# Kernel tuning notes

Measured on AMD Instinct MI355X. Metric: run time of the kernel, lower is better.

## Reference

```python
import jax, jax.numpy as jnp
import numpy as np
from itertools import product

MAX_ALLOC = [3, 3, 3, 3, 3, 3]   # env.maximum_allocation -> 4^6 = 4096 actions
NUM_SESSIONS = 64
STATE_DIM = NUM_SESSIONS + len(MAX_ALLOC)  # 70
HIDDEN = (1024, 1024)
BATCH = 8192


def setup_inputs() -> dict:
    key = jax.random.key(0)
    ks = jax.random.split(key, 8)
    # states: sessions part uniform [0,1); waitlist part uniform [0,4) so mask is nontrivial
    sessions = jax.random.uniform(ks[0], (BATCH, NUM_SESSIONS), dtype=jnp.float32)
    waitlist = jax.random.uniform(ks[1], (BATCH, len(MAX_ALLOC)), dtype=jnp.float32) * 4.0
    states = jnp.concatenate([sessions, waitlist], axis=1)
    # enumerated action space, same order as itertools.product in the torch module
    action_space = jnp.asarray(
        np.array(list(product(*[range(m + 1) for m in MAX_ALLOC])), dtype=np.int32))  # [4096, 6]
    A = action_space.shape[0]
    W1 = jax.random.normal(ks[2], (STATE_DIM, HIDDEN[0]), dtype=jnp.float32) / np.sqrt(STATE_DIM)
    b1 = jnp.zeros((HIDDEN[0],), dtype=jnp.float32)
    W2 = jax.random.normal(ks[3], (HIDDEN[0], HIDDEN[1]), dtype=jnp.float32) / np.sqrt(HIDDEN[0])
    b2 = jnp.zeros((HIDDEN[1],), dtype=jnp.float32)
    Wh = jax.random.normal(ks[4], (HIDDEN[1], A), dtype=jnp.float32) / np.sqrt(HIDDEN[1])
    bh = jnp.zeros((A,), dtype=jnp.float32)
    return {"states": states, "W1": W1, "b1": b1, "W2": W2, "b2": b2,
            "Wh": Wh, "bh": bh, "action_space": action_space,
            "num_sessions": NUM_SESSIONS}


def reference(states, W1, b1, W2, b2, Wh, bh, action_space, num_sessions):
    # vectorized get_action_mask: action j is feasible for row i iff all(action_j <= waitlist_i)
    waitlist = states[:, num_sessions:]                                   # [B, 6]
    feasible = jnp.all(action_space[None, :, :].astype(states.dtype)
                       <= waitlist[:, None, :], axis=-1)                  # [B, A] bool
    mask = feasible.astype(states.dtype)
    # tanh MLP
    h = jnp.tanh(states @ W1 + b1)
    h = jnp.tanh(h @ W2 + b2)
    logits = h @ Wh + bh + jnp.log(mask + 1e-9)                           # [B, A]
    return jax.nn.softmax(logits, axis=1)
```

## Files before the change

kernel.cpp:

```cpp
#include <hip/hip_runtime.h>
#include <hip/hip_bf16.h>
#include <math.h>

using bf16 = __hip_bfloat16;
typedef __attribute__((ext_vector_type(8))) short short8;
typedef __attribute__((ext_vector_type(4))) float f32x4;
typedef __attribute__((ext_vector_type(4))) unsigned int u32x4;

#define BATCH 8192
#define SDIM  70
#define NS    64
#define HID   1024
#define NA    4096
#define KPAD  128

__device__ __forceinline__ void gld_lds16(const bf16* g, bf16* l) {
    __builtin_amdgcn_global_load_lds(
        (const __attribute__((address_space(1))) void*)g,
        (__attribute__((address_space(3))) void*)l, 16, 0, 0);
}

__device__ __forceinline__ short f2bf(float v) {
    union { bf16 b; short s; } u; u.b = __float2bfloat16(v); return u.s;
}

__device__ __forceinline__ void tr32(const float* __restrict__ in, bf16* __restrict__ out,
                                     int K, int N, int Kpad, int bx, int by, int t,
                                     float (*tile)[33]) {
    int kb = by * 32, nb = bx * 32;
    int tx = t & 31, ty = t >> 5;
    #pragma unroll
    for (int i = 0; i < 32; i += 8) {
        int k = kb + ty + i, n = nb + tx;
        tile[ty + i][tx] = (k < K) ? in[(size_t)k * N + n] : 0.0f;
    }
    __syncthreads();
    #pragma unroll
    for (int i = 0; i < 32; i += 8) {
        int n = nb + ty + i, k = kb + tx;
        if (k < Kpad) out[(size_t)n * Kpad + k] = __float2bfloat16(tile[tx][ty + i]);
    }
}

__global__ __launch_bounds__(256)
void prep_k(const float* __restrict__ states, const float* __restrict__ W1,
            const float* __restrict__ W2, const float* __restrict__ Wh,
            const int* __restrict__ act,
            bf16* __restrict__ statesb, bf16* __restrict__ w1bt,
            bf16* __restrict__ w2bt, bf16* __restrict__ whbt,
            unsigned* __restrict__ pact, unsigned* __restrict__ trow) {
    __shared__ float tile[32][33];
    const int b = blockIdx.x, t = threadIdx.x;
    if (b < 512) {
        int idx = b * 256 + t;
        int row = idx >> 4;
        int c0  = (idx & 15) * 8;
        const float* src = states + (size_t)row * SDIM;
        short8 o;
        #pragma unroll
        for (int i = 0; i < 8; i++) {
            int c = c0 + i;
            o[i] = f2bf((c < SDIM) ? src[c] : 0.0f);
        }
        *(short8*)&statesb[(size_t)row * KPAD + c0] = o;
    } else if (b < 640) {
        int r = b - 512;
        tr32(W1, w1bt, SDIM, HID, KPAD, r & 31, r >> 5, t, tile);
    } else if (b < 1664) {
        int r = b - 640;
        tr32(W2, w2bt, HID, HID, HID, r & 31, r >> 5, t, tile);
    } else if (b < 5760) {
        int r = b - 1664;
        tr32(Wh, whbt, HID, NA, HID, r & 127, r >> 7, t, tile);
    } else if (b < 5776) {
        int c = (b - 5760) * 256 + t;
        if (c < NA) {
            const int* a = act + c * 6;
            unsigned p = 0;
            #pragma unroll
            for (int i = 0; i < 6; i++) p |= ((unsigned)a[i]) << (5 * i);
            pact[c] = p;
        }
    } else {
        int row = (b - 5776) * 256 + t;
        const float* wl = states + (size_t)row * SDIM + NS;
        unsigned T = 0;
        #pragma unroll
        for (int i = 0; i < 6; i++) T |= ((unsigned)(int)wl[i]) << (5 * i);
        trow[row] = T;
    }
}

template<int MODE, int BN>
__global__ __launch_bounds__(256)
void gemm128(const bf16* __restrict__ A, const bf16* __restrict__ BT,
             const float* __restrict__ bias, void* __restrict__ Cout,
             int M, int N, int K,
             const unsigned* __restrict__ trow, const unsigned* __restrict__ pact) {
    const int n0 = blockIdx.x * BN;
    const int m0 = blockIdx.y * 128;
    const int tid  = threadIdx.x;
    const int wave = tid >> 6;
    const int lane = tid & 63;

    constexpr int NJ = BN / 32;
    constexpr int BCH = BN / 8;

    __shared__ __align__(16) bf16 As[128 * 64];
    __shared__ __align__(16) bf16 Bs[BN * 64];

    const int lr = lane >> 3;
    const int gk = ((lane & 7) ^ lr) * 8;
    const bf16* ag = A  + (size_t)(m0 + lr) * K + gk;
    const bf16* bg = BT + (size_t)(n0 + lr) * K + gk;

    f32x4 acc[4][NJ];
    #pragma unroll
    for (int i = 0; i < 4; i++)
        #pragma unroll
        for (int j = 0; j < NJ; j++) acc[i][j] = (f32x4){0.f, 0.f, 0.f, 0.f};

    const int rb = (wave >> 1) * 64;
    const int cb = (wave & 1) * (BN / 2);
    const int fr = lane & 15;
    const int kq = lane >> 4;

    int aoff[2][4], boff[2][NJ];
    #pragma unroll
    for (int kk = 0; kk < 2; kk++) {
        const int cbase = kk * 4 + kq;
        #pragma unroll
        for (int i = 0; i < 4; i++) {
            const int ra = rb + i * 16 + fr;
            aoff[kk][i] = (ra * 64 + ((cbase ^ (fr & 7)) * 8)) * 2;
        }
        #pragma unroll
        for (int j = 0; j < NJ; j++) {
            const int rn = cb + j * 16 + fr;
            boff[kk][j] = (rn * 64 + ((cbase ^ (fr & 7)) * 8)) * 2;
        }
    }
    const char* Asb = (const char*)As;
    const char* Bsb = (const char*)Bs;

    for (int k0 = 0; k0 < K; k0 += 64) {
        #pragma unroll
        for (int q = 0; q < 4; q++) {
            const int ch = q * 4 + wave;
            gld_lds16(ag + (size_t)(ch * 8) * K + k0, &As[ch * 512]);
            if (ch < BCH)
                gld_lds16(bg + (size_t)(ch * 8) * K + k0, &Bs[ch * 512]);
        }
        __syncthreads();

        #pragma unroll
        for (int kk = 0; kk < 2; kk++) {
            short8 af[4], bfr[NJ];
            #pragma unroll
            for (int i = 0; i < 4; i++)  af[i]  = *(const short8*)(Asb + aoff[kk][i]);
            #pragma unroll
            for (int j = 0; j < NJ; j++) bfr[j] = *(const short8*)(Bsb + boff[kk][j]);
            #pragma unroll
            for (int i = 0; i < 4; i++)
                #pragma unroll
                for (int j = 0; j < NJ; j++)
                    acc[i][j] = __builtin_amdgcn_mfma_f32_16x16x32_bf16(af[i], bfr[j], acc[i][j], 0, 0, 0);
        }
        __syncthreads();
    }

    const int orow = m0 + rb + (lane >> 4) * 4;
    const int ocol = n0 + cb + fr;
    float bv[NJ];
    #pragma unroll
    for (int j = 0; j < NJ; j++) bv[j] = bias[ocol + j * 16];
    unsigned pv[NJ];
    if (MODE == 3) {
        #pragma unroll
        for (int j = 0; j < NJ; j++) pv[j] = pact[ocol + j * 16];
    }
    const unsigned H = 0x21084210u;
    #pragma unroll
    for (int i = 0; i < 4; i++) {
        #pragma unroll
        for (int r = 0; r < 4; r++) {
            const int row = orow + i * 16 + r;
            unsigned TH = 0;
            if (MODE == 3) TH = trow[row] | H;
            #pragma unroll
            for (int j = 0; j < NJ; j++) {
                float val = acc[i][j][r] + bv[j];
                const size_t off = (size_t)row * N + ocol + j * 16;
                if (MODE == 0) {
                    ((bf16*)Cout)[off] = __float2bfloat16(tanhf(val));
                } else if (MODE == 1) {
                    ((float*)Cout)[off] = val;
                } else if (MODE == 3) {
                    if (((TH - pv[j]) & H) != H) val -= 20.7232658f;
                    ((bf16*)Cout)[off] = __float2bfloat16(val);
                } else {
                    ((bf16*)Cout)[off] = __float2bfloat16(val);
                }
            }
        }
    }
}

__global__ __launch_bounds__(256)
void softmax_k(const bf16* __restrict__ logitsb, float* __restrict__ out) {
    const int row  = (blockIdx.x << 2) | (threadIdx.x >> 6);
    const int lane = threadIdx.x & 63;

    const unsigned* lrow = (const unsigned*)(logitsb + (size_t)row * NA);

    float v[64];
    float s = 0.f;
    #pragma unroll
    for (int c = 0; c < 8; c++) {
        u32x4 raw = *(const u32x4*)(lrow + c * 256 + lane * 4);
        #pragma unroll
        for (int e = 0; e < 4; e++) {
            float lo = __expf(__uint_as_float(raw[e] << 16));
            float hi = __expf(__uint_as_float(raw[e] & 0xffff0000u));
            v[c * 8 + 2 * e]     = lo;
            v[c * 8 + 2 * e + 1] = hi;
            s += lo + hi;
        }
    }
    #pragma unroll
    for (int o = 32; o > 0; o >>= 1) s += __shfl_xor(s, o, 64);
    const float inv = 1.0f / s;

    float* orow = out + (size_t)row * NA;
    #pragma unroll
    for (int c = 0; c < 8; c++) {
        const int fbase = c * 512 + lane * 8;
        #pragma unroll
        for (int q = 0; q < 2; q++) {
            f32x4 o4 = { v[c * 8 + q * 4] * inv,     v[c * 8 + q * 4 + 1] * inv,
                         v[c * 8 + q * 4 + 2] * inv, v[c * 8 + q * 4 + 3] * inv };
            *(f32x4*)(orow + fbase + q * 4) = o4;
        }
    }
}

extern "C" void kernel_launch(void* const* d_in, const int* in_sizes, int n_in,
                              void* d_out, int out_size, void* d_ws, size_t ws_size,
                              hipStream_t stream) {
    const float* states = (const float*)d_in[0];
    const float* W1 = (const float*)d_in[1];
    const float* b1 = (const float*)d_in[2];
    const float* W2 = (const float*)d_in[3];
    const float* b2 = (const float*)d_in[4];
    const float* Wh = (const float*)d_in[5];
    const float* bh = (const float*)d_in[6];
    const int*   act = (const int*)d_in[7];
    float* out = (float*)d_out;

    char* ws = (char*)d_ws;
    bf16* statesb = (bf16*)ws; ws += (size_t)BATCH * KPAD * 2;
    bf16* w1bt    = (bf16*)ws; ws += (size_t)HID * KPAD * 2;
    bf16* w2bt    = (bf16*)ws; ws += (size_t)HID * HID * 2;
    bf16* whbt    = (bf16*)ws; ws += (size_t)NA * HID * 2;
    bf16* h1      = (bf16*)ws; ws += (size_t)BATCH * HID * 2;
    bf16* h2      = (bf16*)ws; ws += (size_t)BATCH * HID * 2;
    bf16* logitsb = (bf16*)ws; ws += (size_t)BATCH * NA * 2;
    unsigned* pact = (unsigned*)ws; ws += (size_t)NA * 4;
    unsigned* trow = (unsigned*)ws; ws += (size_t)BATCH * 4;

    prep_k<<<5808, 256, 0, stream>>>(states, W1, W2, Wh, act,
                                     statesb, w1bt, w2bt, whbt, pact, trow);

    gemm128<0, 64><<<dim3(HID / 64, BATCH / 128), 256, 0, stream>>>(
        statesb, w1bt, b1, h1, BATCH, HID, KPAD, nullptr, nullptr);
    gemm128<0, 64><<<dim3(HID / 64, BATCH / 128), 256, 0, stream>>>(
        h1, w2bt, b2, h2, BATCH, HID, HID, nullptr, nullptr);
    gemm128<3, 128><<<dim3(NA / 128, BATCH / 128), 256, 0, stream>>>(
        h2, whbt, bh, logitsb, BATCH, NA, HID, trow, pact);

    softmax_k<<<BATCH / 4, 256, 0, stream>>>(logitsb, out);
}
```

Measured before the change: 294.6 us.

## Double-buffer GEMM LDS tiles with K=32 stages and new swizzle

Replaces the single-buffered K=64 LDS tiling with double-buffered K=32 stages, so the next tile's global-to-LDS loads are issued before the current tile's MFMAs. This drops one barrier per iteration and aims to overlap memory latency with compute. The shared layout and XOR swizzle are rebuilt for 32-wide rows, and each GEMM gets its own wrapper kernel. Halving K per stage doubles the number of barriers per unit of work, and the prefetch into the other buffer may race with waves still reading it unless the async LDS loads are properly waited on.

```diff
diff --git a/kernel.cpp b/kernel.cpp
--- a/kernel.cpp
+++ b/kernel.cpp
@@ -92,27 +92,27 @@
 }
 
 template<int MODE, int BN>
-__global__ __launch_bounds__(256)
-void gemm128(const bf16* __restrict__ A, const bf16* __restrict__ BT,
-             const float* __restrict__ bias, void* __restrict__ Cout,
-             int M, int N, int K,
-             const unsigned* __restrict__ trow, const unsigned* __restrict__ pact) {
+__device__ __forceinline__
+void gemm_body(const bf16* __restrict__ A, const bf16* __restrict__ BT,
+               const float* __restrict__ bias, void* __restrict__ Cout,
+               int M, int N, int K,
+               const unsigned* __restrict__ trow, const unsigned* __restrict__ pact) {
     const int n0 = blockIdx.x * BN;
     const int m0 = blockIdx.y * 128;
     const int tid  = threadIdx.x;
     const int wave = tid >> 6;
     const int lane = tid & 63;
 
-    constexpr int NJ = BN / 32;
-    constexpr int BCH = BN / 8;
-
-    __shared__ __align__(16) bf16 As[128 * 64];
-    __shared__ __align__(16) bf16 Bs[BN * 64];
-
-    const int lr = lane >> 3;
-    const int gk = ((lane & 7) ^ lr) * 8;
-    const bf16* ag = A  + (size_t)(m0 + lr) * K + gk;
-    const bf16* bg = BT + (size_t)(n0 + lr) * K + gk;
+    constexpr int NJ  = BN / 32;
+    constexpr int BCH = BN / 16;
+
+    __shared__ __align__(16) bf16 As[2][128 * 32];
+    __shared__ __align__(16) bf16 Bs[2][BN * 32];
+
+    const int lrr = lane >> 2;
+    const int gkc = ((lane & 3) ^ ((lane >> 3) & 3)) * 8;
+    const bf16* ag = A  + (size_t)(m0 + lrr) * K + gkc;
+    const bf16* bg = BT + (size_t)(n0 + lrr) * K + gkc;
 
     f32x4 acc[4][NJ];
     #pragma unroll
@@ -125,48 +125,45 @@
     const int fr = lane & 15;
     const int kq = lane >> 4;
 
-    int aoff[2][4], boff[2][NJ];
-    #pragma unroll
-    for (int kk = 0; kk < 2; kk++) {
-        const int cbase = kk * 4 + kq;
-        #pragma unroll
-        for (int i = 0; i < 4; i++) {
-            const int ra = rb + i * 16 + fr;
-            aoff[kk][i] = (ra * 64 + ((cbase ^ (fr & 7)) * 8)) * 2;
-        }
-        #pragma unroll
-        for (int j = 0; j < NJ; j++) {
-            const int rn = cb + j * 16 + fr;
-            boff[kk][j] = (rn * 64 + ((cbase ^ (fr & 7)) * 8)) * 2;
-        }
-    }
-    const char* Asb = (const char*)As;
-    const char* Bsb = (const char*)Bs;
-
-    for (int k0 = 0; k0 < K; k0 += 64) {
-        #pragma unroll
-        for (int q = 0; q < 4; q++) {
+    const int sl = (kq ^ ((fr >> 1) & 3)) * 16;
+    int aoff[4], boff[NJ];
+    #pragma unroll
+    for (int i = 0; i < 4; i++)  aoff[i] = (rb + i * 16 + fr) * 64 + sl;
+    #pragma unroll
+    for (int j = 0; j < NJ; j++) boff[j] = (cb + j * 16 + fr) * 64 + sl;
+
+    const int NT = K >> 5;
+
+    auto STAGE = [&](int b, int k0) {
+        #pragma unroll
+        for (int q = 0; q < 2; q++) {
             const int ch = q * 4 + wave;
-            gld_lds16(ag + (size_t)(ch * 8) * K + k0, &As[ch * 512]);
+            gld_lds16(ag + (size_t)(ch * 16) * K + k0, &As[b][ch * 512]);
             if (ch < BCH)
-                gld_lds16(bg + (size_t)(ch * 8) * K + k0, &Bs[ch * 512]);
-        }
+                gld_lds16(bg + (size_t)(ch * 16) * K + k0, &Bs[b][ch * 512]);
+        }
+    };
+
+    STAGE(0, 0);
+    __syncthreads();
+
+    int buf = 0;
+    for (int t = 0; t < NT; t++) {
+        if (t + 1 < NT) STAGE(buf ^ 1, (t + 1) * 32);
+        const char* Asb = (const char*)&As[buf][0];
+        const char* Bsb = (const char*)&Bs[buf][0];
+        short8 af[4], bfr[NJ];
+        #pragma unroll
+        for (int i = 0; i < 4; i++)  af[i]  = *(const short8*)(Asb + aoff[i]);
+        #pragma unroll
+        for (int j = 0; j < NJ; j++) bfr[j] = *(const short8*)(Bsb + boff[j]);
+        #pragma unroll
+        for (int i = 0; i < 4; i++)
+            #pragma unroll
+            for (int j = 0; j < NJ; j++)
+                acc[i][j] = __builtin_amdgcn_mfma_f32_16x16x32_bf16(af[i], bfr[j], acc[i][j], 0, 0, 0);
         __syncthreads();
-
-        #pragma unroll
-        for (int kk = 0; kk < 2; kk++) {
-            short8 af[4], bfr[NJ];
-            #pragma unroll
-            for (int i = 0; i < 4; i++)  af[i]  = *(const short8*)(Asb + aoff[kk][i]);
-            #pragma unroll
-            for (int j = 0; j < NJ; j++) bfr[j] = *(const short8*)(Bsb + boff[kk][j]);
-            #pragma unroll
-            for (int i = 0; i < 4; i++)
-                #pragma unroll
-                for (int j = 0; j < NJ; j++)
-                    acc[i][j] = __builtin_amdgcn_mfma_f32_16x16x32_bf16(af[i], bfr[j], acc[i][j], 0, 0, 0);
-        }
-        __syncthreads();
+        buf ^= 1;
     }
 
     const int orow = m0 + rb + (lane >> 4) * 4;
@@ -193,8 +190,6 @@
                 const size_t off = (size_t)row * N + ocol + j * 16;
                 if (MODE == 0) {
                     ((bf16*)Cout)[off] = __float2bfloat16(tanhf(val));
-                } else if (MODE == 1) {
-                    ((float*)Cout)[off] = val;
                 } else if (MODE == 3) {
                     if (((TH - pv[j]) & H) != H) val -= 20.7232658f;
                     ((bf16*)Cout)[off] = __float2bfloat16(val);
@@ -204,6 +199,23 @@
             }
         }
     }
+}
+
+__global__ __launch_bounds__(256)
+void g1_gemm(const bf16* __restrict__ A, const bf16* __restrict__ BT,
+             const float* __restrict__ bias, void* __restrict__ C, int M, int N, int K) {
+    gemm_body<0, 64>(A, BT, bias, C, M, N, K, nullptr, nullptr);
+}
+__global__ __launch_bounds__(256)
+void g2_gemm(const bf16* __restrict__ A, const bf16* __restrict__ BT,
+             const float* __restrict__ bias, void* __restrict__ C, int M, int N, int K) {
+    gemm_body<0, 64>(A, BT, bias, C, M, N, K, nullptr, nullptr);
+}
+__global__ __launch_bounds__(256)
+void g3_gemm(const bf16* __restrict__ A, const bf16* __restrict__ BT,
+             const float* __restrict__ bias, void* __restrict__ C, int M, int N, int K,
+             const unsigned* __restrict__ trow, const unsigned* __restrict__ pact) {
+    gemm_body<3, 128>(A, BT, bias, C, M, N, K, trow, pact);
 }
 
 __global__ __launch_bounds__(256)
@@ -271,11 +283,11 @@
     prep_k<<<5808, 256, 0, stream>>>(states, W1, W2, Wh, act,
                                      statesb, w1bt, w2bt, whbt, pact, trow);
 
-    gemm128<0, 64><<<dim3(HID / 64, BATCH / 128), 256, 0, stream>>>(
-        statesb, w1bt, b1, h1, BATCH, HID, KPAD, nullptr, nullptr);
-    gemm128<0, 64><<<dim3(HID / 64, BATCH / 128), 256, 0, stream>>>(
-        h1, w2bt, b2, h2, BATCH, HID, HID, nullptr, nullptr);
-    gemm128<3, 128><<<dim3(NA / 128, BATCH / 128), 256, 0, stream>>>(
+    g1_gemm<<<dim3(HID / 64, BATCH / 128), 256, 0, stream>>>(
+        statesb, w1bt, b1, h1, BATCH, HID, KPAD);
+    g2_gemm<<<dim3(HID / 64, BATCH / 128), 256, 0, stream>>>(
+        h1, w2bt, b2, h2, BATCH, HID, HID);
+    g3_gemm<<<dim3(NA / 128, BATCH / 128), 256, 0, stream>>>(
         h2, whbt, bh, logitsb, BATCH, NA, HID, trow, pact);
 
     softmax_k<<<BATCH / 4, 256, 0, stream>>>(logitsb, out);
```

Measured after the change: 318.4 us. 8.1% more time.
